# Kernel tuning notes

Hardware: AMD Instinct MI355X
Metric: run time of the kernel (lower is better)

## Reference

```python
import jax, jax.numpy as jnp
import numpy as np

EMBED = 1024
HEADS = 16
HEAD_DIM = EMBED // HEADS
WINDOW = 256

def _linear(x, W, b):
    # torch nn.Linear: y = x @ W.T + b, W shape (out, in)
    return jnp.einsum('bse,oe->bso', x, W) + b

def setup_inputs() -> dict:
    key = jax.random.key(0)
    ks = jax.random.split(key, 16)
    B, S = 2, 2048
    std = 1.0 / np.sqrt(EMBED)
    d = {
        'query': jax.random.normal(ks[0], (B, S, EMBED), jnp.float32),
        'key':   jax.random.normal(ks[1], (B, S, EMBED), jnp.float32),
        'value': jax.random.normal(ks[2], (B, S, EMBED), jnp.float32),
        'Wq': jax.random.normal(ks[3], (EMBED, EMBED), jnp.float32) * std,
        'bq': jnp.zeros((EMBED,), jnp.float32),
        'Wk': jax.random.normal(ks[4], (EMBED, EMBED), jnp.float32) * std,
        'bk': jnp.zeros((EMBED,), jnp.float32),
        'Wv': jax.random.normal(ks[5], (EMBED, EMBED), jnp.float32) * std,
        'bv': jnp.zeros((EMBED,), jnp.float32),
        'Wo': jax.random.normal(ks[6], (EMBED, EMBED), jnp.float32) * std,
        'bo': jnp.zeros((EMBED,), jnp.float32),
    }
    return d

def reference(query, key, value, Wq, bq, Wk, bk, Wv, bv, Wo, bo):
    B, S, E = query.shape
    q = _linear(query, Wq, bq)
    k = _linear(key, Wk, bk)
    v = _linear(value, Wv, bv)
    # (B, H, S, D)
    q = q.reshape(B, S, HEADS, HEAD_DIM).transpose(0, 2, 1, 3)
    k = k.reshape(B, S, HEADS, HEAD_DIM).transpose(0, 2, 1, 3)
    v = v.reshape(B, S, HEADS, HEAD_DIM).transpose(0, 2, 1, 3)
    scale = 1.0 / jnp.sqrt(jnp.asarray(HEAD_DIM, q.dtype))
    scores = jnp.einsum('bhqd,bhkd->bhqk', q, k) * scale
    # Faithful local masking: mask is 0 inside window [i-w//2, i+w//2], 1 outside,
    # and is ADDED to scores (as in the source, not -inf fill).
    i = jnp.arange(S)[:, None]
    j = jnp.arange(S)[None, :]
    half = WINDOW // 2
    band = (jnp.abs(i - j) <= half)
    add_mask = jnp.where(band, 0.0, 1.0).astype(scores.dtype)  # (S, S)
    scores = scores + add_mask[None, None, :, :]
    attn = jax.nn.softmax(scores, axis=-1)  # dropout = identity (eval)
    out = jnp.einsum('bhqk,bhkd->bhqd', attn, v)
    out = out.transpose(0, 2, 1, 3).reshape(B, S, E)
    return _linear(out, Wo, bo)
```

## Files before the change

kernel.cpp:

```cpp
#include <hip/hip_runtime.h>
#include <stdint.h>

#define B_ 2
#define S_ 2048
#define E_ 1024
#define H_ 16
#define D_ 64
#define M_ (B_*S_)
#define PROJ_ ((size_t)M_*E_)
#define HALF_W 128

typedef float    f32x4 __attribute__((ext_vector_type(4)));
typedef short    s16x8 __attribute__((ext_vector_type(8)));
typedef __bf16   bf16x8 __attribute__((ext_vector_type(8)));
typedef _Float16 f16x8 __attribute__((ext_vector_type(8)));
typedef unsigned int u32x4 __attribute__((ext_vector_type(4)));

typedef const __attribute__((address_space(1))) void* gas_t;
typedef __attribute__((address_space(3))) void*       las_t;

__device__ __forceinline__ void gl16(const void* g, void* l) {
    __builtin_amdgcn_global_load_lds((gas_t)g, (las_t)l, 16, 0, 0);
}

__device__ __forceinline__ f32x4 MFMA(bf16x8 a, bf16x8 b, f32x4 c) {
    return __builtin_amdgcn_mfma_f32_16x16x32_bf16(a, b, c, 0, 0, 0);
}
__device__ __forceinline__ f32x4 MFMAH(f16x8 a, f16x8 b, f32x4 c) {
    return __builtin_amdgcn_mfma_f32_16x16x32_f16(a, b, c, 0, 0, 0);
}

__device__ __forceinline__ unsigned short f2bf(float f) {
    union { float f; unsigned int u; } x; x.f = f;
    unsigned int u = x.u + 0x7FFFu + ((x.u >> 16) & 1u);
    return (unsigned short)(u >> 16);
}

__device__ __forceinline__ s16x8 cvt8(f32x4 a, f32x4 b) {
    s16x8 h;
    h[0]=(short)f2bf(a[0]); h[1]=(short)f2bf(a[1]); h[2]=(short)f2bf(a[2]); h[3]=(short)f2bf(a[3]);
    h[4]=(short)f2bf(b[0]); h[5]=(short)f2bf(b[1]); h[6]=(short)f2bf(b[2]); h[7]=(short)f2bf(b[3]);
    return h;
}

__global__ __launch_bounds__(256) void cvt_kernel(
    const float* __restrict__ q, const float* __restrict__ k, const float* __restrict__ v,
    const float* __restrict__ Wq, const float* __restrict__ Wk,
    const float* __restrict__ Wv, const float* __restrict__ Wo,
    unsigned short* __restrict__ xq, unsigned short* __restrict__ xk,
    unsigned short* __restrict__ xv, unsigned short* __restrict__ wbf)
{
    const int z = blockIdx.y;
    if (z >= 3 && blockIdx.x >= 512) return;
    const float* src; unsigned short* dst;
    switch (z) {
        case 0: src = q;  dst = xq; break;
        case 1: src = k;  dst = xk; break;
        case 2: src = v;  dst = xv; break;
        case 3: src = Wq; dst = wbf; break;
        case 4: src = Wk; dst = wbf + (size_t)E_*E_; break;
        case 5: src = Wv; dst = wbf + 2*(size_t)E_*E_; break;
        default: src = Wo; dst = wbf + 3*(size_t)E_*E_; break;
    }
    size_t i = ((size_t)blockIdx.x * 256 + threadIdx.x) * 8;
    f32x4 a = *(const f32x4*)(src + i);
    f32x4 c = *(const f32x4*)(src + i + 4);
    *(s16x8*)(dst + i) = cvt8(a, c);
}

__global__ __launch_bounds__(256, 2) void qkv_kernel(
    const unsigned short* __restrict__ xq, const unsigned short* __restrict__ xk,
    const unsigned short* __restrict__ xv,
    const unsigned short* __restrict__ wbf,
    const float* __restrict__ Wq, const float* __restrict__ Wk, const float* __restrict__ Wv,
    const float* __restrict__ bq, const float* __restrict__ bk, const float* __restrict__ bv,
    unsigned short* __restrict__ qkvout)
{
    const int z = blockIdx.z;
    const unsigned short* X  = (z==0) ? xq : (z==1) ? xk : xv;
    const float*          Bf = (z==0) ? Wq : (z==1) ? Wk : Wv;
    const float*        bias = (z==0) ? bq : (z==1) ? bk : bv;
    const unsigned short* Bbf = wbf ? (wbf + (size_t)z * E_ * E_) : nullptr;
    unsigned short* dst = qkvout + (size_t)z * PROJ_;

    __shared__ __align__(16) unsigned short As[2][128 * 32];
    __shared__ __align__(16) unsigned short Bs[2][128 * 32];

    const int t = threadIdx.x;
    const int lane = t & 63, w = t >> 6;
    const int quad = lane >> 4, l16 = lane & 15;
    const int wm = (w & 1) * 64, wn = (w >> 1) * 64;
    const int rowBase = blockIdx.y * 128, nBase = blockIdx.x * 128;

    const int r0 = t >> 2;
    const int c4 = (t & 3) ^ (r0 & 3);
    const unsigned short* gA  = X + (size_t)(rowBase + r0) * E_ + c4 * 8;
    const unsigned short* gBb = Bbf ? Bbf + (size_t)(nBase + r0) * E_ + c4 * 8 : nullptr;
    const float*          gBf = Bf + (size_t)(nBase + r0) * E_ + c4 * 8;

    f32x4 acc[4][4] = {};

    auto issue = [&](int kk, int pb) {
        unsigned short* dA = &As[pb][(size_t)w * 512];
        gl16(gA + kk, dA);
        gl16(gA + (size_t)64 * E_ + kk, dA + 2048);
        if (gBb) {
            unsigned short* dB = &Bs[pb][(size_t)w * 512];
            gl16(gBb + kk, dB);
            gl16(gBb + (size_t)64 * E_ + kk, dB + 2048);
        } else {
            const float* gp0 = gBf + kk;
            const float* gp1 = gBf + (size_t)64 * E_ + kk;
            f32x4 a0 = *(const f32x4*)gp0, a1 = *(const f32x4*)(gp0 + 4);
            f32x4 b0 = *(const f32x4*)gp1, b1 = *(const f32x4*)(gp1 + 4);
            *(s16x8*)&Bs[pb][(size_t)r0 * 32 + (t & 3) * 8]        = cvt8(a0, a1);
            *(s16x8*)&Bs[pb][(size_t)(r0 + 64) * 32 + (t & 3) * 8] = cvt8(b0, b1);
        }
    };

    issue(0, 0);
    __syncthreads();

    for (int s = 0; s < 32; s++) {
        const int pb = s & 1;
        if (s < 31) issue((s + 1) * 32, pb ^ 1);

        bf16x8 af[4], bfr[4];
        #pragma unroll
        for (int im = 0; im < 4; im++) {
            int r = wm + im * 16 + l16;
            af[im] = *(const bf16x8*)&As[pb][(size_t)r * 32 + ((quad ^ (l16 & 3)) * 8)];
        }
        #pragma unroll
        for (int in = 0; in < 4; in++) {
            int r = wn + in * 16 + l16;
            bfr[in] = *(const bf16x8*)&Bs[pb][(size_t)r * 32 + ((quad ^ (l16 & 3)) * 8)];
        }
        #pragma unroll
        for (int im = 0; im < 4; im++)
            #pragma unroll
            for (int in = 0; in < 4; in++)
                acc[im][in] = MFMA(af[im], bfr[in], acc[im][in]);
        __syncthreads();
    }

    #pragma unroll
    for (int im = 0; im < 4; im++)
      #pragma unroll
      for (int in = 0; in < 4; in++) {
        int col = nBase + wn + in * 16 + l16;
        float bb = bias[col];
        int h = col >> 6, d = col & 63;
        #pragma unroll
        for (int r = 0; r < 4; r++) {
            int row = rowBase + wm + im * 16 + quad * 4 + r;
            float val = acc[im][in][r] + bb;
            int b = row >> 11, s = row & 2047;
            size_t base = ((size_t)(b * H_ + h)) * ((size_t)S_ * D_);
            if (z == 0) {
                dst[base + (size_t)s * D_ + d] = f2bf(val);
            } else if (z == 1) {
                dst[base + (size_t)s * D_ + d] = f2bf(val * 0.1803368801111204f);
            } else {
                int k6 = s & 63;
                int slot = ((k6 >> 5) & 1) * 32 + ((k6 >> 2) & 3) * 8
                         + ((k6 >> 4) & 1) * 4 + (k6 & 3);
                _Float16 hv = (_Float16)val;
                dst[base + (size_t)d * S_ + (s & ~63) + slot] =
                    __builtin_bit_cast(unsigned short, hv);
            }
        }
      }
}

__global__ __launch_bounds__(256, 4) void attn_kernel(
    const unsigned short* __restrict__ qkvout, unsigned short* __restrict__ attnout)
{
    const int bh = blockIdx.y, b = bh >> 4, h = bh & 15;
    const int qbase = blockIdx.x * 64;
    const int t = threadIdx.x, w = t >> 6, lane = t & 63;
    const int quad = lane >> 4, l16 = lane & 15;

    const unsigned short* qg = qkvout + (size_t)bh * (S_ * D_);
    const unsigned short* kg = qkvout + PROJ_ + (size_t)bh * (S_ * D_);
    const unsigned short* vT = qkvout + 2 * PROJ_ + (size_t)bh * (S_ * D_);

    __shared__ __align__(16) unsigned short Ks [2][64 * 64];
    __shared__ __align__(16) unsigned short VTs[2][64 * 64];

    const int qi = qbase + w * 16 + l16;
    bf16x8 aq0 = *(const bf16x8*)&qg[(size_t)qi * 64 + quad * 8];
    bf16x8 aq1 = *(const bf16x8*)&qg[(size_t)qi * 64 + 32 + quad * 8];

    f32x4 Oi[4] = {}, Oo[4] = {};
    f32x4 Si = {}, So = {};

    const int r0 = t >> 3;
    const int ch = ((t & 7) ^ (r0 & 7)) * 8;

    f16x8 onesv;
    #pragma unroll
    for (int j = 0; j < 8; j++) onesv[j] = (_Float16)1.0f;

    auto issue = [&](int kt, int pb) {
        unsigned short* dK = &Ks [pb][(size_t)w * 512];
        unsigned short* dV = &VTs[pb][(size_t)w * 512];
        gl16(kg + (size_t)(kt + r0) * 64 + ch,      dK);
        gl16(kg + (size_t)(kt + r0 + 32) * 64 + ch, dK + 2048);
        gl16(vT + (size_t)r0 * S_ + kt + ch,        dV);
        gl16(vT + (size_t)(r0 + 32) * S_ + kt + ch, dV + 2048);
    };

    issue(0, 0);
    __syncthreads();

    for (int s = 0; s < 32; s++) {
        const int pb = s & 1;
        const int kt = s * 64;
        if (s < 31) issue(kt + 64, pb ^ 1);

        const int dq = qbase - kt;
        const int adq = dq < 0 ? -dq : dq;
        const int cls = (adq <= 64) ? 0 : (adq >= 192 ? 1 : 2);

        f32x4 pp[4];
        const int sw = l16 & 7;
        #pragma unroll
        for (int sub = 0; sub < 4; sub++) {
            int row = sub * 16 + l16;
            bf16x8 bk0 = *(const bf16x8*)&Ks[pb][(size_t)row * 64 + ((quad ^ sw) * 8)];
            bf16x8 bk1 = *(const bf16x8*)&Ks[pb][(size_t)row * 64 + (((4 + quad) ^ sw) * 8)];
            f32x4 zz = {};
            zz = MFMA(bk0, aq0, zz);
            zz = MFMA(bk1, aq1, zz);
            if (cls == 2) {
                const int jb = kt + sub * 16 + quad * 4;
                #pragma unroll
                for (int r = 0; r < 4; r++) {
                    int di = qi - (jb + r); di = di < 0 ? -di : di;
                    pp[sub][r] = exp2f(zz[r] + (di <= HALF_W ? 0.f : 1.44269504089f));
                }
            } else {
                #pragma unroll
                for (int r = 0; r < 4; r++) pp[sub][r] = exp2f(zz[r]);
            }
        }

        u32x4 u0, u1;
        u0[0] = __builtin_bit_cast(unsigned int, __builtin_amdgcn_cvt_pkrtz(pp[0][0], pp[0][1]));
        u0[1] = __builtin_bit_cast(unsigned int, __builtin_amdgcn_cvt_pkrtz(pp[0][2], pp[0][3]));
        u0[2] = __builtin_bit_cast(unsigned int, __builtin_amdgcn_cvt_pkrtz(pp[1][0], pp[1][1]));
        u0[3] = __builtin_bit_cast(unsigned int, __builtin_amdgcn_cvt_pkrtz(pp[1][2], pp[1][3]));
        u1[0] = __builtin_bit_cast(unsigned int, __builtin_amdgcn_cvt_pkrtz(pp[2][0], pp[2][1]));
        u1[1] = __builtin_bit_cast(unsigned int, __builtin_amdgcn_cvt_pkrtz(pp[2][2], pp[2][3]));
        u1[2] = __builtin_bit_cast(unsigned int, __builtin_amdgcn_cvt_pkrtz(pp[3][0], pp[3][1]));
        u1[3] = __builtin_bit_cast(unsigned int, __builtin_amdgcn_cvt_pkrtz(pp[3][2], pp[3][3]));
        f16x8 aP0 = __builtin_bit_cast(f16x8, u0);
        f16x8 aP1 = __builtin_bit_cast(f16x8, u1);

        if (cls == 1) {
            #pragma unroll
            for (int dt = 0; dt < 4; dt++) {
                int row = dt * 16 + l16;
                f16x8 v0 = *(const f16x8*)&VTs[pb][(size_t)row * 64 + ((quad ^ sw) * 8)];
                f16x8 v1 = *(const f16x8*)&VTs[pb][(size_t)row * 64 + (((4 + quad) ^ sw) * 8)];
                Oo[dt] = MFMAH(aP0, v0, Oo[dt]);
                Oo[dt] = MFMAH(aP1, v1, Oo[dt]);
            }
            So = MFMAH(aP0, onesv, So);
            So = MFMAH(aP1, onesv, So);
        } else {
            #pragma unroll
            for (int dt = 0; dt < 4; dt++) {
                int row = dt * 16 + l16;
                f16x8 v0 = *(const f16x8*)&VTs[pb][(size_t)row * 64 + ((quad ^ sw) * 8)];
                f16x8 v1 = *(const f16x8*)&VTs[pb][(size_t)row * 64 + (((4 + quad) ^ sw) * 8)];
                Oi[dt] = MFMAH(aP0, v0, Oi[dt]);
                Oi[dt] = MFMAH(aP1, v1, Oi[dt]);
            }
            Si = MFMAH(aP0, onesv, Si);
            Si = MFMAH(aP1, onesv, Si);
        }
        __syncthreads();
    }

    const float E1 = 2.718281828459045f;
    float rd[4];
    #pragma unroll
    for (int r = 0; r < 4; r++) rd[r] = 1.0f / (Si[r] + E1 * So[r]);
    #pragma unroll
    for (int dt = 0; dt < 4; dt++)
        #pragma unroll
        for (int r = 0; r < 4; r++) {
            float oo = (Oi[dt][r] + E1 * Oo[dt][r]) * rd[r];
            int srow2 = qbase + w * 16 + quad * 4 + r;
            int col   = h * 64 + dt * 16 + l16;
            attnout[((size_t)(b * S_ + srow2)) * E_ + col] = f2bf(oo);
        }
}

__global__ __launch_bounds__(256, 2) void oproj_kernel(
    const unsigned short* __restrict__ Aattn, const unsigned short* __restrict__ WoBf,
    const float* __restrict__ Wo, const float* __restrict__ bo, float* __restrict__ out)
{
    __shared__ __align__(16) unsigned short As[2][64 * 32];
    __shared__ __align__(16) unsigned short Bs[2][128 * 32];

    const int t = threadIdx.x;
    const int lane = t & 63, w = t >> 6;
    const int quad = lane >> 4, l16 = lane & 15;
    const int wm = (w & 1) * 32, wn = (w >> 1) * 64;
    const int rowBase = blockIdx.y * 64, nBase = blockIdx.x * 128;

    const int r0 = t >> 2;
    const int c4 = (t & 3) ^ (r0 & 3);
    const unsigned short* gA  = Aattn + (size_t)(rowBase + r0) * E_ + c4 * 8;
    const unsigned short* gBb = WoBf ? WoBf + (size_t)(nBase + r0) * E_ + c4 * 8 : nullptr;
    const float*          gBf = Wo + (size_t)(nBase + r0) * E_ + c4 * 8;

    f32x4 acc[2][4] = {};

    auto issue = [&](int kk, int pb) {
        gl16(gA + kk, &As[pb][(size_t)w * 512]);
        if (gBb) {
            unsigned short* dB = &Bs[pb][(size_t)w * 512];
            gl16(gBb + kk, dB);
            gl16(gBb + (size_t)64 * E_ + kk, dB + 2048);
        } else {
            const float* gp0 = gBf + kk;
            const float* gp1 = gBf + (size_t)64 * E_ + kk;
            f32x4 a0 = *(const f32x4*)gp0, a1 = *(const f32x4*)(gp0 + 4);
            f32x4 b0 = *(const f32x4*)gp1, b1 = *(const f32x4*)(gp1 + 4);
            *(s16x8*)&Bs[pb][(size_t)r0 * 32 + (t & 3) * 8]        = cvt8(a0, a1);
            *(s16x8*)&Bs[pb][(size_t)(r0 + 64) * 32 + (t & 3) * 8] = cvt8(b0, b1);
        }
    };

    issue(0, 0);
    __syncthreads();

    for (int s = 0; s < 32; s++) {
        const int pb = s & 1;
        if (s < 31) issue((s + 1) * 32, pb ^ 1);

        bf16x8 af[2], bfr[4];
        #pragma unroll
        for (int im = 0; im < 2; im++) {
            int r = wm + im * 16 + l16;
            af[im] = *(const bf16x8*)&As[pb][(size_t)r * 32 + ((quad ^ (l16 & 3)) * 8)];
        }
        #pragma unroll
        for (int in = 0; in < 4; in++) {
            int r = wn + in * 16 + l16;
            bfr[in] = *(const bf16x8*)&Bs[pb][(size_t)r * 32 + ((quad ^ (l16 & 3)) * 8)];
        }
        #pragma unroll
        for (int im = 0; im < 2; im++)
            #pragma unroll
            for (int in = 0; in < 4; in++)
                acc[im][in] = MFMA(af[im], bfr[in], acc[im][in]);
        __syncthreads();
    }

    #pragma unroll
    for (int im = 0; im < 2; im++)
      #pragma unroll
      for (int in = 0; in < 4; in++) {
          int col = nBase + wn + in * 16 + l16;
          float bb = bo[col];
          #pragma unroll
          for (int r = 0; r < 4; r++) {
              int row = rowBase + wm + im * 16 + quad * 4 + r;
              out[(size_t)row * E_ + col] = acc[im][in][r] + bb;
          }
      }
}

extern "C" void kernel_launch(void* const* d_in, const int* in_sizes, int n_in,
                              void* d_out, int out_size, void* d_ws, size_t ws_size,
                              hipStream_t stream) {
    const float* query = (const float*)d_in[0];
    const float* key_  = (const float*)d_in[1];
    const float* value = (const float*)d_in[2];
    const float* Wq = (const float*)d_in[3];
    const float* bq = (const float*)d_in[4];
    const float* Wk = (const float*)d_in[5];
    const float* bk = (const float*)d_in[6];
    const float* Wv = (const float*)d_in[7];
    const float* bv = (const float*)d_in[8];
    const float* Wo = (const float*)d_in[9];
    const float* bo = (const float*)d_in[10];

    unsigned short* ws      = (unsigned short*)d_ws;
    unsigned short* xv      = ws;
    unsigned short* attnout = ws;
    unsigned short* qkvout  = ws + PROJ_;
    size_t needW = (4 * PROJ_ + 4 * (size_t)E_ * E_) * 2;
    unsigned short* wbf = (ws_size >= needW) ? (ws + 4 * PROJ_) : nullptr;
    unsigned short* xq = (unsigned short*)d_out;
    unsigned short* xk = xq + PROJ_;

    cvt_kernel<<<dim3(2048, wbf ? 7 : 3), 256, 0, stream>>>(
        query, key_, value, Wq, Wk, Wv, Wo, xq, xk, xv, wbf);
    qkv_kernel<<<dim3(8, 32, 3), 256, 0, stream>>>(
        xq, xk, xv, wbf, Wq, Wk, Wv, bq, bk, bv, qkvout);
    attn_kernel<<<dim3(32, 32), 256, 0, stream>>>(qkvout, attnout);
    oproj_kernel<<<dim3(8, 64), 256, 0, stream>>>(
        attnout, wbf ? wbf + 3 * (size_t)E_ * E_ : nullptr, Wo, bo, (float*)d_out);
}
```

Before: 240.4 us.

## Swap QKV GEMM operands for vectorized epilogue stores and blocked V layout

The QKV projection now puts the weight tile in the MFMA A operand and the activations in B. Each lane then holds four consecutive output features for one sequence position, so Q and K are written as 4-wide vector stores with a single vectorized bias load instead of scattered 2-byte stores. V is stored in a per-64-key blocked transpose (key block, head dim, slot), which the attention kernel reads as contiguous 64-element rows. Launch bounds are raised from 2 to 3 blocks per CU, which tightens the register budget and may cause spills.

```diff
diff --git a/kernel.cpp b/kernel.cpp
--- a/kernel.cpp
+++ b/kernel.cpp
@@ -11,6 +11,7 @@
 #define HALF_W 128
 
 typedef float    f32x4 __attribute__((ext_vector_type(4)));
+typedef short    s16x4 __attribute__((ext_vector_type(4)));
 typedef short    s16x8 __attribute__((ext_vector_type(8)));
 typedef __bf16   bf16x8 __attribute__((ext_vector_type(8)));
 typedef _Float16 f16x8 __attribute__((ext_vector_type(8)));
@@ -68,7 +69,7 @@
     *(s16x8*)(dst + i) = cvt8(a, c);
 }
 
-__global__ __launch_bounds__(256, 2) void qkv_kernel(
+__global__ __launch_bounds__(256, 3) void qkv_kernel(
     const unsigned short* __restrict__ xq, const unsigned short* __restrict__ xk,
     const unsigned short* __restrict__ xv,
     const unsigned short* __restrict__ wbf,
@@ -78,9 +79,9 @@
 {
     const int z = blockIdx.z;
     const unsigned short* X  = (z==0) ? xq : (z==1) ? xk : xv;
-    const float*          Bf = (z==0) ? Wq : (z==1) ? Wk : Wv;
+    const float*          Wf = (z==0) ? Wq : (z==1) ? Wk : Wv;
     const float*        bias = (z==0) ? bq : (z==1) ? bk : bv;
-    const unsigned short* Bbf = wbf ? (wbf + (size_t)z * E_ * E_) : nullptr;
+    const unsigned short* Wb = wbf ? (wbf + (size_t)z * E_ * E_) : nullptr;
     unsigned short* dst = qkvout + (size_t)z * PROJ_;
 
     __shared__ __align__(16) unsigned short As[2][128 * 32];
@@ -89,32 +90,32 @@
     const int t = threadIdx.x;
     const int lane = t & 63, w = t >> 6;
     const int quad = lane >> 4, l16 = lane & 15;
-    const int wm = (w & 1) * 64, wn = (w >> 1) * 64;
-    const int rowBase = blockIdx.y * 128, nBase = blockIdx.x * 128;
+    const int wo = (w & 1) * 64, wsb = (w >> 1) * 64;
+    const int oBase = blockIdx.x * 128, sBase = blockIdx.y * 128;
 
     const int r0 = t >> 2;
     const int c4 = (t & 3) ^ (r0 & 3);
-    const unsigned short* gA  = X + (size_t)(rowBase + r0) * E_ + c4 * 8;
-    const unsigned short* gBb = Bbf ? Bbf + (size_t)(nBase + r0) * E_ + c4 * 8 : nullptr;
-    const float*          gBf = Bf + (size_t)(nBase + r0) * E_ + c4 * 8;
+    const unsigned short* gX  = X + (size_t)(sBase + r0) * E_ + c4 * 8;
+    const unsigned short* gWb = Wb ? Wb + (size_t)(oBase + r0) * E_ + c4 * 8 : nullptr;
+    const float*          gWf = Wf + (size_t)(oBase + r0) * E_ + c4 * 8;
 
     f32x4 acc[4][4] = {};
 
     auto issue = [&](int kk, int pb) {
-        unsigned short* dA = &As[pb][(size_t)w * 512];
-        gl16(gA + kk, dA);
-        gl16(gA + (size_t)64 * E_ + kk, dA + 2048);
-        if (gBb) {
-            unsigned short* dB = &Bs[pb][(size_t)w * 512];
-            gl16(gBb + kk, dB);
-            gl16(gBb + (size_t)64 * E_ + kk, dB + 2048);
+        unsigned short* dB = &Bs[pb][(size_t)w * 512];
+        gl16(gX + kk, dB);
+        gl16(gX + (size_t)64 * E_ + kk, dB + 2048);
+        if (gWb) {
+            unsigned short* dA = &As[pb][(size_t)w * 512];
+            gl16(gWb + kk, dA);
+            gl16(gWb + (size_t)64 * E_ + kk, dA + 2048);
         } else {
-            const float* gp0 = gBf + kk;
-            const float* gp1 = gBf + (size_t)64 * E_ + kk;
+            const float* gp0 = gWf + kk;
+            const float* gp1 = gWf + (size_t)64 * E_ + kk;
             f32x4 a0 = *(const f32x4*)gp0, a1 = *(const f32x4*)(gp0 + 4);
             f32x4 b0 = *(const f32x4*)gp1, b1 = *(const f32x4*)(gp1 + 4);
-            *(s16x8*)&Bs[pb][(size_t)r0 * 32 + (t & 3) * 8]        = cvt8(a0, a1);
-            *(s16x8*)&Bs[pb][(size_t)(r0 + 64) * 32 + (t & 3) * 8] = cvt8(b0, b1);
+            *(s16x8*)&As[pb][(size_t)r0 * 32 + (t & 3) * 8]        = cvt8(a0, a1);
+            *(s16x8*)&As[pb][(size_t)(r0 + 64) * 32 + (t & 3) * 8] = cvt8(b0, b1);
         }
     };
 
@@ -127,50 +128,58 @@
 
         bf16x8 af[4], bfr[4];
         #pragma unroll
-        for (int im = 0; im < 4; im++) {
-            int r = wm + im * 16 + l16;
-            af[im] = *(const bf16x8*)&As[pb][(size_t)r * 32 + ((quad ^ (l16 & 3)) * 8)];
-        }
-        #pragma unroll
-        for (int in = 0; in < 4; in++) {
-            int r = wn + in * 16 + l16;
-            bfr[in] = *(const bf16x8*)&Bs[pb][(size_t)r * 32 + ((quad ^ (l16 & 3)) * 8)];
-        }
-        #pragma unroll
-        for (int im = 0; im < 4; im++)
+        for (int io = 0; io < 4; io++) {
+            int r = wo + io * 16 + l16;
+            af[io] = *(const bf16x8*)&As[pb][(size_t)r * 32 + ((quad ^ (l16 & 3)) * 8)];
+        }
+        #pragma unroll
+        for (int is = 0; is < 4; is++) {
+            int r = wsb + is * 16 + l16;
+            bfr[is] = *(const bf16x8*)&Bs[pb][(size_t)r * 32 + ((quad ^ (l16 & 3)) * 8)];
+        }
+        #pragma unroll
+        for (int io = 0; io < 4; io++)
             #pragma unroll
-            for (int in = 0; in < 4; in++)
-                acc[im][in] = MFMA(af[im], bfr[in], acc[im][in]);
+            for (int is = 0; is < 4; is++)
+                acc[io][is] = MFMA(af[io], bfr[is], acc[io][is]);
         __syncthreads();
     }
 
+    const float KSCL = 0.1803368801111204f;
     #pragma unroll
-    for (int im = 0; im < 4; im++)
-      #pragma unroll
-      for (int in = 0; in < 4; in++) {
-        int col = nBase + wn + in * 16 + l16;
-        float bb = bias[col];
-        int h = col >> 6, d = col & 63;
-        #pragma unroll
-        for (int r = 0; r < 4; r++) {
-            int row = rowBase + wm + im * 16 + quad * 4 + r;
-            float val = acc[im][in][r] + bb;
-            int b = row >> 11, s = row & 2047;
+    for (int is = 0; is < 4; is++) {
+        int sg = sBase + wsb + is * 16 + l16;
+        int b = sg >> 11, sg2 = sg & 2047;
+        int k6 = sg2 & 63;
+        int slot = ((k6 >> 5) & 1) * 32 + ((k6 >> 2) & 3) * 8
+                 + ((k6 >> 4) & 1) * 4 + (k6 & 3);
+        #pragma unroll
+        for (int io = 0; io < 4; io++) {
+            int ocol0 = oBase + wo + io * 16 + quad * 4;
+            f32x4 bias4 = *(const f32x4*)&bias[ocol0];
+            int h = ocol0 >> 6, d0 = ocol0 & 63;
             size_t base = ((size_t)(b * H_ + h)) * ((size_t)S_ * D_);
             if (z == 0) {
-                dst[base + (size_t)s * D_ + d] = f2bf(val);
+                s16x4 h4;
+                #pragma unroll
+                for (int r = 0; r < 4; r++) h4[r] = (short)f2bf(acc[io][is][r] + bias4[r]);
+                *(s16x4*)&dst[base + (size_t)sg2 * D_ + d0] = h4;
             } else if (z == 1) {
-                dst[base + (size_t)s * D_ + d] = f2bf(val * 0.1803368801111204f);
+                s16x4 h4;
+                #pragma unroll
+                for (int r = 0; r < 4; r++)
+                    h4[r] = (short)f2bf((acc[io][is][r] + bias4[r]) * KSCL);
+                *(s16x4*)&dst[base + (size_t)sg2 * D_ + d0] = h4;
             } else {
-                int k6 = s & 63;
-                int slot = ((k6 >> 5) & 1) * 32 + ((k6 >> 2) & 3) * 8
-                         + ((k6 >> 4) & 1) * 4 + (k6 & 3);
-                _Float16 hv = (_Float16)val;
-                dst[base + (size_t)d * S_ + (s & ~63) + slot] =
-                    __builtin_bit_cast(unsigned short, hv);
+                size_t vb = base + (size_t)(sg2 >> 6) * 4096 + (size_t)d0 * 64 + slot;
+                #pragma unroll
+                for (int r = 0; r < 4; r++) {
+                    _Float16 hv = (_Float16)(acc[io][is][r] + bias4[r]);
+                    dst[vb + (size_t)r * 64] = __builtin_bit_cast(unsigned short, hv);
+                }
             }
         }
-      }
+    }
 }
 
 __global__ __launch_bounds__(256, 4) void attn_kernel(
@@ -207,8 +216,8 @@
         unsigned short* dV = &VTs[pb][(size_t)w * 512];
         gl16(kg + (size_t)(kt + r0) * 64 + ch,      dK);
         gl16(kg + (size_t)(kt + r0 + 32) * 64 + ch, dK + 2048);
-        gl16(vT + (size_t)r0 * S_ + kt + ch,        dV);
-        gl16(vT + (size_t)(r0 + 32) * S_ + kt + ch, dV + 2048);
+        gl16(vT + (size_t)(kt + r0) * 64 + ch,      dV);
+        gl16(vT + (size_t)(kt + r0 + 32) * 64 + ch, dV + 2048);
     };
 
     issue(0, 0);
```

New measurement: 238.0 us. No clear change (-1.0%).
